# Optimization experiments

Measured on AMD Instinct MI355X. Metric: run time of the kernel, lower is better.

## Reference

```python
import jax, jax.numpy as jnp
import numpy as np

N = 50000      # nodes
E_RAND = 600000  # random edges per meta-path
M = 3          # meta-paths
D_IN = 128
D_OUT = 128
H_SEM = 128    # SemanticAttention hidden (default 128)
NEG_SLOPE = 0.2  # DGL GATConv leaky_relu default


def setup_inputs() -> dict:
    key = jax.random.key(0)
    ks = jax.random.split(key, 12)
    h = jax.random.normal(ks[0], (N, D_IN), dtype=jnp.float32)
    src = jax.random.randint(ks[1], (M, E_RAND), 0, N, dtype=jnp.int32)
    dst = jax.random.randint(ks[2], (M, E_RAND), 0, N, dtype=jnp.int32)
    # add self-loops (dgl.add_self_loop): guarantees every dst has >=1 edge
    loops = jnp.broadcast_to(jnp.arange(N, dtype=jnp.int32), (M, N))
    edge_src = jnp.concatenate([src, loops], axis=1)
    edge_dst = jnp.concatenate([dst, loops], axis=1)
    W_gat = jax.random.normal(ks[3], (M, D_IN, D_OUT), dtype=jnp.float32) * 0.05
    attn_l = jax.random.normal(ks[4], (M, D_OUT), dtype=jnp.float32) * 0.1
    attn_r = jax.random.normal(ks[5], (M, D_OUT), dtype=jnp.float32) * 0.1
    bias_gat = jax.random.normal(ks[6], (M, D_OUT), dtype=jnp.float32) * 0.02
    Ws1 = jax.random.normal(ks[7], (D_OUT, H_SEM), dtype=jnp.float32) * 0.05
    bs1 = jnp.zeros((H_SEM,), dtype=jnp.float32)
    Ws2 = jax.random.normal(ks[8], (H_SEM,), dtype=jnp.float32) * 0.05
    return {"h": h, "edge_src": edge_src, "edge_dst": edge_dst,
            "W_gat": W_gat, "attn_l": attn_l, "attn_r": attn_r,
            "bias_gat": bias_gat, "Ws1": Ws1, "bs1": bs1, "Ws2": Ws2}


def _gat_meta_path(feat_m, el_m, er_m, src, dst):
    # feat_m: [N, D]; el/er: [N]; src/dst: [E]
    e = jax.nn.leaky_relu(el_m[src] + er_m[dst], NEG_SLOPE)  # [E]
    emax = jax.ops.segment_max(e, dst, num_segments=N)       # [N]
    ex = jnp.exp(e - emax[dst])
    denom = jax.ops.segment_sum(ex, dst, num_segments=N)     # [N]
    a = ex / denom[dst]                                      # edge softmax
    # scatter-aggregate weighted source features -> [N, D]
    return jax.ops.segment_sum(a[:, None] * feat_m[src], dst, num_segments=N)


def reference(h, edge_src, edge_dst, W_gat, attn_l, attn_r, bias_gat, Ws1, bs1, Ws2):
    # per-meta-path GATConv projections
    feat = jnp.einsum('ni,mio->mno', h, W_gat)            # [M, N, D]
    el = jnp.einsum('mno,mo->mn', feat, attn_l)           # [M, N]
    er = jnp.einsum('mno,mo->mn', feat, attn_r)           # [M, N]
    z = jax.vmap(_gat_meta_path)(feat, el, er, edge_src, edge_dst)  # [M, N, D]
    z = jax.nn.elu(z + bias_gat[:, None, :])              # GATConv bias + activation
    z = jnp.transpose(z, (1, 0, 2))                       # [N, M, D]
    # SemanticAttention: Linear -> tanh -> Linear(no bias), mean over nodes, softmax over meta-paths
    w = jnp.einsum('nmh,h->nm', jnp.tanh(jnp.einsum('nmd,dh->nmh', z, Ws1) + bs1), Ws2)
    beta = jax.nn.softmax(w.mean(0))                      # [M]
    return jnp.einsum('m,nmd->nd', beta, z)               # [N, D]
```

## Files before the change

kernel.cpp:

```cpp
#include <hip/hip_runtime.h>
#include <hip/hip_fp16.h>

#define NV 50000
#define EE 650000
#define MM 3
#define NBUK 49
#define CHSZ 4096
#define NCH 159
#define SEMBLK 586

typedef __attribute__((ext_vector_type(8))) __bf16 bf16x8;
typedef __attribute__((ext_vector_type(8))) unsigned short u16x8;
typedef __attribute__((ext_vector_type(4))) float f32x4;

__device__ __forceinline__ unsigned short f2bf(float f) {
    unsigned u = __builtin_bit_cast(unsigned, f);
    u += 0x7FFFu + ((u >> 16) & 1u);
    return (unsigned short)(u >> 16);
}
__device__ __forceinline__ float bflo(unsigned v) {
    unsigned x = v << 16; return __builtin_bit_cast(float, x);
}
__device__ __forceinline__ float bfhi(unsigned v) {
    unsigned x = v & 0xFFFF0000u; return __builtin_bit_cast(float, x);
}
__device__ __forceinline__ bf16x8 zero8() {
    u16x8 u = {0,0,0,0,0,0,0,0};
    return __builtin_bit_cast(bf16x8, u);
}

__global__ void prep_wt(const float* __restrict__ Wg, const float* __restrict__ Ws1,
                        unsigned short* __restrict__ WT, unsigned short* __restrict__ WsT) {
    int idx = blockIdx.x * 256 + threadIdx.x;
    if (idx < MM * 16384) {
        int m = idx / 16384, r = idx % 16384;
        int o = r >> 7, d = r & 127;
        WT[idx] = f2bf(Wg[m * 16384 + d * 128 + o]);
    } else {
        int r = idx - MM * 16384;
        int j = r >> 7, d = r & 127;
        WsT[r] = f2bf(Ws1[d * 128 + j]);
    }
}

__global__ void prep_h(const float* __restrict__ h, unsigned* __restrict__ hb) {
    int idx = blockIdx.x * 256 + threadIdx.x;
    if (idx < NV * 64) {
        float2 f = *reinterpret_cast<const float2*>(h + (size_t)idx * 2);
        hb[idx] = ((unsigned)f2bf(f.x)) | (((unsigned)f2bf(f.y)) << 16);
    }
}

__global__ __launch_bounds__(256, 2) void gemm_feat(
    const unsigned short* __restrict__ hb, const unsigned short* __restrict__ WT,
    const float* __restrict__ attn_l, const float* __restrict__ attn_r,
    unsigned* __restrict__ featb, float* __restrict__ el, float* __restrict__ er) {
    const int m = blockIdx.y;
    const int tid = threadIdx.x;
    const int wave = tid >> 6, lane = tid & 63;
    const int lo = lane & 15, hi = lane >> 4;
    const int rowbase = blockIdx.x * 256 + wave * 64;
    const unsigned short* WTm = WT + m * 16384;

    f32x4 acc[4][8];
#pragma unroll
    for (int a = 0; a < 4; ++a)
#pragma unroll
        for (int b = 0; b < 8; ++b) acc[a][b] = (f32x4){0.f, 0.f, 0.f, 0.f};

#pragma unroll
    for (int kk = 0; kk < 4; ++kk) {
        bf16x8 bfrag[8];
#pragma unroll
        for (int ct = 0; ct < 8; ++ct)
            bfrag[ct] = *reinterpret_cast<const bf16x8*>(WTm + (ct * 16 + lo) * 128 + kk * 32 + hi * 8);
#pragma unroll
        for (int rt = 0; rt < 4; ++rt) {
            int row = rowbase + rt * 16 + lo;
            bf16x8 af = (row < NV)
                ? *reinterpret_cast<const bf16x8*>(hb + (size_t)row * 128 + kk * 32 + hi * 8)
                : zero8();
#pragma unroll
            for (int ct = 0; ct < 8; ++ct)
                acc[rt][ct] = __builtin_amdgcn_mfma_f32_16x16x32_bf16(af, bfrag[ct], acc[rt][ct], 0, 0, 0);
        }
    }

    float alv[8], arv[8];
#pragma unroll
    for (int ct = 0; ct < 8; ++ct) {
        alv[ct] = attn_l[m * 128 + ct * 16 + lo];
        arv[ct] = attn_r[m * 128 + ct * 16 + lo];
    }

#pragma unroll
    for (int rt = 0; rt < 4; ++rt) {
        float pl[4] = {0.f, 0.f, 0.f, 0.f}, pr[4] = {0.f, 0.f, 0.f, 0.f};
#pragma unroll
        for (int ct = 0; ct < 8; ++ct)
#pragma unroll
            for (int i = 0; i < 4; ++i) {
                pl[i] += acc[rt][ct][i] * alv[ct];
                pr[i] += acc[rt][ct][i] * arv[ct];
            }
#pragma unroll
        for (int s = 1; s < 16; s <<= 1)
#pragma unroll
            for (int i = 0; i < 4; ++i) {
                pl[i] += __shfl_xor(pl[i], s, 64);
                pr[i] += __shfl_xor(pr[i], s, 64);
            }
        int row0 = rowbase + rt * 16 + hi * 4;
        if (lo == 0) {
#pragma unroll
            for (int i = 0; i < 4; ++i)
                if (row0 + i < NV) {
                    el[m * NV + row0 + i] = pl[i];
                    er[m * NV + row0 + i] = pr[i];
                }
        }
#pragma unroll
        for (int ct = 0; ct < 8; ++ct)
#pragma unroll
            for (int i = 0; i < 4; ++i) {
                float v = acc[rt][ct][i];
                float vp = __shfl_xor(v, 1, 64);
                int row = row0 + i;
                if (((lo & 1) == 0) && row < NV) {
                    unsigned pk = ((unsigned)f2bf(v)) | (((unsigned)f2bf(vp)) << 16);
                    featb[(size_t)(m * NV + row) * 64 + ct * 8 + (lo >> 1)] = pk;
                }
            }
    }
}

__global__ __launch_bounds__(256) void hist_k(const int* __restrict__ edst,
                                              int* __restrict__ counts) {
    int m = blockIdx.y, c = blockIdx.x, tid = threadIdx.x;
    __shared__ int hsm[NBUK];
    if (tid < NBUK) hsm[tid] = 0;
    __syncthreads();
    int base = c * CHSZ;
#pragma unroll
    for (int i = 0; i < CHSZ / 256; ++i) {
        int e = base + i * 256 + tid;
        if (e < EE) {
            int d = edst[(size_t)m * EE + e];
            atomicAdd(&hsm[d >> 10], 1);
        }
    }
    __syncthreads();
    if (tid < NBUK) counts[(m * NCH + c) * NBUK + tid] = hsm[tid];
}

__global__ __launch_bounds__(256) void scan_k(const int* __restrict__ counts,
                                              int* __restrict__ chunkpos,
                                              int* __restrict__ bstart) {
    int t = threadIdx.x;
    __shared__ int btot[MM * NBUK];
    if (t < MM * NBUK) {
        int m = t / NBUK, b = t % NBUK;
        int run = 0;
        for (int c = 0; c < NCH; ++c) {
            chunkpos[(m * NCH + c) * NBUK + b] = run;
            run += counts[(m * NCH + c) * NBUK + b];
        }
        btot[t] = run;
    }
    __syncthreads();
    if (t == 0) {
        for (int m = 0; m < MM; ++m) {
            int run = 0;
            for (int b = 0; b < NBUK; ++b) {
                bstart[m * NBUK + b] = run;
                run += btot[m * NBUK + b];
            }
        }
    }
}

__global__ __launch_bounds__(256) void scat1_k(const int* __restrict__ esrc,
                                               const int* __restrict__ edst,
                                               const int* __restrict__ chunkpos,
                                               const int* __restrict__ bstart,
                                               unsigned* __restrict__ staging) {
    int m = blockIdx.y, c = blockIdx.x, tid = threadIdx.x;
    __shared__ int cnt[NBUK];
    __shared__ int sofs[NBUK];
    if (tid < NBUK) {
        cnt[tid] = 0;
        sofs[tid] = bstart[m * NBUK + tid] + chunkpos[(m * NCH + c) * NBUK + tid];
    }
    __syncthreads();
    int base = c * CHSZ;
#pragma unroll
    for (int i = 0; i < CHSZ / 256; ++i) {
        int e = base + i * 256 + tid;
        if (e < EE) {
            int s = esrc[(size_t)m * EE + e];
            int d = edst[(size_t)m * EE + e];
            int b = d >> 10;
            int r = atomicAdd(&cnt[b], 1);
            staging[(size_t)m * EE + sofs[b] + r] =
                ((unsigned)(d & 1023) << 16) | (unsigned)s;
        }
    }
}

__global__ __launch_bounds__(1024) void bsort_k(const unsigned* __restrict__ staging,
                                                const int* __restrict__ bstart,
                                                const float* __restrict__ el,
                                                const float* __restrict__ er,
                                                unsigned* __restrict__ csr,
                                                int* __restrict__ start,
                                                int* __restrict__ deg) {
    int b = blockIdx.x, m = blockIdx.y, t = threadIdx.x;
    __shared__ int hsm[1024];
    __shared__ int sc[1024];
    __shared__ int cur[1024];
    hsm[t] = 0;
    __syncthreads();
    int sbase = bstart[m * NBUK + b];
    int nseg = ((b == NBUK - 1) ? EE : bstart[m * NBUK + b + 1]) - sbase;
    const unsigned* sp = staging + (size_t)m * EE + sbase;
    for (int i = t; i < nseg; i += 1024)
        atomicAdd(&hsm[sp[i] >> 16], 1);
    __syncthreads();
    int v = hsm[t];
    sc[t] = v;
    __syncthreads();
#pragma unroll
    for (int s = 1; s < 1024; s <<= 1) {
        int add = (t >= s) ? sc[t - s] : 0;
        __syncthreads();
        sc[t] += add;
        __syncthreads();
    }
    int excl = sc[t] - v;
    cur[t] = excl;
    int node = (b << 10) + t;
    if (node < NV) {
        deg[m * NV + node] = v;
        start[m * NV + node] = sbase + excl;
    }
    __syncthreads();
    unsigned* cp = csr + (size_t)m * EE + sbase;
    int node0 = b << 10;
    for (int i = t; i < nseg; i += 1024) {
        unsigned rec = sp[i];
        int dloc = rec >> 16;
        int s = rec & 0xFFFF;
        float x = el[m * NV + s] + er[m * NV + node0 + dloc];
        x = x > 0.f ? x : 0.2f * x;
        float ex = __expf(x);
        unsigned short hx = __builtin_bit_cast(unsigned short, __float2half(ex));
        int slot = atomicAdd(&cur[dloc], 1);
        cp[slot] = ((unsigned)hx << 16) | (unsigned)s;
    }
}

__global__ __launch_bounds__(256) void aggregate_k(
    const unsigned* __restrict__ featb, const unsigned* __restrict__ csr,
    const int* __restrict__ start, const int* __restrict__ deg,
    const float* __restrict__ bias, float* __restrict__ z, unsigned* __restrict__ zb) {
    int gw = blockIdx.x * 4 + (threadIdx.x >> 6);
    int lane = threadIdx.x & 63;
    int m = gw / NV;
    int st = start[gw];
    int dg = deg[gw];
    const unsigned* pp = csr + (size_t)m * EE + st;
    const unsigned* fb = featb + (size_t)m * NV * 64 + lane;
    float2 acc = {0.f, 0.f};
    float den = 0.f;
    int full = dg & ~7;
    int e0 = 0;
    for (; e0 < full; e0 += 8) {
        unsigned p[8];
#pragma unroll
        for (int i = 0; i < 8; ++i) p[i] = pp[e0 + i];
        unsigned v[8];
#pragma unroll
        for (int i = 0; i < 8; ++i) v[i] = fb[(size_t)(p[i] & 0xFFFF) * 64];
#pragma unroll
        for (int i = 0; i < 8; ++i) {
            float x = __half2float(__builtin_bit_cast(__half, (unsigned short)(p[i] >> 16)));
            acc.x += x * bflo(v[i]); acc.y += x * bfhi(v[i]);
            den += x;
        }
    }
    if (e0 < dg) {
        int dgm1 = dg - 1;
        unsigned p[8];
#pragma unroll
        for (int i = 0; i < 8; ++i) p[i] = pp[min(e0 + i, dgm1)];
        unsigned v[8];
#pragma unroll
        for (int i = 0; i < 8; ++i) v[i] = fb[(size_t)(p[i] & 0xFFFF) * 64];
#pragma unroll
        for (int i = 0; i < 8; ++i) {
            float x = (e0 + i < dg)
                ? __half2float(__builtin_bit_cast(__half, (unsigned short)(p[i] >> 16))) : 0.f;
            acc.x += x * bflo(v[i]); acc.y += x * bfhi(v[i]);
            den += x;
        }
    }
    float inv = 1.f / den;
    int d0 = lane * 2;
    float z0 = acc.x * inv + bias[m * 128 + d0];
    float z1 = acc.y * inv + bias[m * 128 + d0 + 1];
    z0 = z0 > 0.f ? z0 : (__expf(z0) - 1.f);
    z1 = z1 > 0.f ? z1 : (__expf(z1) - 1.f);
    float2 o = {z0, z1};
    *reinterpret_cast<float2*>(z + (size_t)gw * 128 + d0) = o;
    zb[(size_t)gw * 64 + lane] = ((unsigned)f2bf(z0)) | (((unsigned)f2bf(z1)) << 16);
}

__global__ __launch_bounds__(256, 2) void semantic_k(
    const unsigned* __restrict__ zb, const unsigned short* __restrict__ WsT,
    const float* __restrict__ bs1, const float* __restrict__ Ws2,
    float* __restrict__ wpart) {
    const int tid = threadIdx.x;
    const int wave = tid >> 6, lane = tid & 63;
    const int lo = lane & 15, hi = lane >> 4;
    const int rowbase = blockIdx.x * 256 + wave * 64;

    f32x4 acc[4][8];
#pragma unroll
    for (int a = 0; a < 4; ++a)
#pragma unroll
        for (int b = 0; b < 8; ++b) acc[a][b] = (f32x4){0.f, 0.f, 0.f, 0.f};

#pragma unroll
    for (int kk = 0; kk < 4; ++kk) {
        bf16x8 bfrag[8];
#pragma unroll
        for (int ct = 0; ct < 8; ++ct)
            bfrag[ct] = *reinterpret_cast<const bf16x8*>(WsT + (ct * 16 + lo) * 128 + kk * 32 + hi * 8);
#pragma unroll
        for (int rt = 0; rt < 4; ++rt) {
            int row = rowbase + rt * 16 + lo;
            bf16x8 af = (row < MM * NV)
                ? *reinterpret_cast<const bf16x8*>(zb + (size_t)row * 64 + kk * 16 + hi * 2)
                : zero8();
#pragma unroll
            for (int ct = 0; ct < 8; ++ct)
                acc[rt][ct] = __builtin_amdgcn_mfma_f32_16x16x32_bf16(af, bfrag[ct], acc[rt][ct], 0, 0, 0);
        }
    }

    float w2v[8], b1v[8];
#pragma unroll
    for (int ct = 0; ct < 8; ++ct) {
        w2v[ct] = Ws2[ct * 16 + lo];
        b1v[ct] = bs1[ct * 16 + lo];
    }

    float t0 = 0.f, t1 = 0.f, t2 = 0.f;
#pragma unroll
    for (int rt = 0; rt < 4; ++rt) {
        int rbase = rowbase + rt * 16;
        if (rbase >= MM * NV) continue;
        int mm = rbase / NV;
        float p = 0.f;
#pragma unroll
        for (int ct = 0; ct < 8; ++ct)
#pragma unroll
            for (int i = 0; i < 4; ++i) {
                float x = acc[rt][ct][i] + b1v[ct];
                x = fminf(fmaxf(x, -15.f), 15.f);
                float t = __expf(2.f * x);
                p += w2v[ct] * ((t - 1.f) / (t + 1.f));
            }
#pragma unroll
        for (int s = 1; s < 64; s <<= 1) p += __shfl_xor(p, s, 64);
        if (mm == 0) t0 += p; else if (mm == 1) t1 += p; else t2 += p;
    }

    __shared__ float smw[4][3];
    if (lane == 0) { smw[wave][0] = t0; smw[wave][1] = t1; smw[wave][2] = t2; }
    __syncthreads();
    if (tid < 3)
        wpart[blockIdx.x * 4 + tid] =
            smw[0][tid] + smw[1][tid] + smw[2][tid] + smw[3][tid];
}

__global__ __launch_bounds__(64) void beta_k(const float* __restrict__ wpart,
                                             float* __restrict__ beta) {
    int lane = threadIdx.x;
    float t0 = 0.f, t1 = 0.f, t2 = 0.f;
    for (int b = lane; b < SEMBLK; b += 64) {
        t0 += wpart[b * 4 + 0];
        t1 += wpart[b * 4 + 1];
        t2 += wpart[b * 4 + 2];
    }
#pragma unroll
    for (int s = 1; s < 64; s <<= 1) {
        t0 += __shfl_xor(t0, s, 64);
        t1 += __shfl_xor(t1, s, 64);
        t2 += __shfl_xor(t2, s, 64);
    }
    if (lane == 0) {
        float w0 = t0 * (1.f / NV), w1 = t1 * (1.f / NV), w2 = t2 * (1.f / NV);
        float mx = fmaxf(w0, fmaxf(w1, w2));
        float e0 = __expf(w0 - mx), e1 = __expf(w1 - mx), e2 = __expf(w2 - mx);
        float inv = 1.f / (e0 + e1 + e2);
        beta[0] = e0 * inv; beta[1] = e1 * inv; beta[2] = e2 * inv;
    }
}

__global__ __launch_bounds__(256) void combine_k(const float* __restrict__ z,
                                                 const float* __restrict__ beta,
                                                 float* __restrict__ out) {
    size_t base = (size_t)(blockIdx.x * 256 + threadIdx.x) * 4;
    float b0 = beta[0], b1 = beta[1], b2 = beta[2];
    float4 z0 = *reinterpret_cast<const float4*>(z + base);
    float4 z1 = *reinterpret_cast<const float4*>(z + (size_t)NV * 128 + base);
    float4 z2 = *reinterpret_cast<const float4*>(z + (size_t)2 * NV * 128 + base);
    float4 o;
    o.x = b0 * z0.x + b1 * z1.x + b2 * z2.x;
    o.y = b0 * z0.y + b1 * z1.y + b2 * z2.y;
    o.z = b0 * z0.z + b1 * z1.z + b2 * z2.z;
    o.w = b0 * z0.w + b1 * z1.w + b2 * z2.w;
    *reinterpret_cast<float4*>(out + base) = o;
}

extern "C" void kernel_launch(void* const* d_in, const int* in_sizes, int n_in,
                              void* d_out, int out_size, void* d_ws, size_t ws_size,
                              hipStream_t stream) {
    const float* h      = (const float*)d_in[0];
    const int*   esrc   = (const int*)d_in[1];
    const int*   edst   = (const int*)d_in[2];
    const float* Wg     = (const float*)d_in[3];
    const float* attn_l = (const float*)d_in[4];
    const float* attn_r = (const float*)d_in[5];
    const float* bias   = (const float*)d_in[6];
    const float* Ws1    = (const float*)d_in[7];
    const float* bs1    = (const float*)d_in[8];
    const float* Ws2    = (const float*)d_in[9];
    float* out = (float*)d_out;

    char* w = (char*)d_ws;
    auto alloc = [&](size_t bytes) { char* p = w; w += (bytes + 255) & ~(size_t)255; return p; };
    unsigned short* WT   = (unsigned short*)alloc((size_t)MM * 128 * 128 * 2);
    unsigned short* WsT  = (unsigned short*)alloc((size_t)128 * 128 * 2);
    unsigned* hb    = (unsigned*)alloc((size_t)NV * 64 * 4);
    unsigned* featb = (unsigned*)alloc((size_t)MM * NV * 64 * 4);
    unsigned* zbp   = (unsigned*)alloc((size_t)MM * NV * 64 * 4);
    float* zbuf   = (float*)alloc((size_t)MM * NV * 128 * 4);
    float* el     = (float*)alloc((size_t)MM * NV * 4);
    float* er     = (float*)alloc((size_t)MM * NV * 4);
    int*   deg    = (int*)alloc((size_t)MM * NV * 4);
    int*   startb = (int*)alloc((size_t)MM * NV * 4);
    int*   counts = (int*)alloc((size_t)MM * NCH * NBUK * 4);
    int*   chunkpos = (int*)alloc((size_t)MM * NCH * NBUK * 4);
    int*   bstart = (int*)alloc((size_t)MM * NBUK * 4);
    unsigned* staging = (unsigned*)alloc((size_t)MM * EE * 4);
    unsigned* csr     = (unsigned*)alloc((size_t)MM * EE * 4);
    float* wpart  = (float*)alloc((size_t)SEMBLK * 4 * 4);
    float* beta   = (float*)alloc(256);

    hipLaunchKernelGGL(prep_wt, dim3(256), dim3(256), 0, stream, Wg, Ws1, WT, WsT);
    hipLaunchKernelGGL(prep_h, dim3((NV * 64 + 255) / 256), dim3(256), 0, stream, h, hb);
    hipLaunchKernelGGL(gemm_feat, dim3(196, MM), dim3(256), 0, stream,
                       (const unsigned short*)hb, WT, attn_l, attn_r, featb, el, er);
    hipLaunchKernelGGL(hist_k, dim3(NCH, MM), dim3(256), 0, stream, edst, counts);
    hipLaunchKernelGGL(scan_k, dim3(1), dim3(256), 0, stream, counts, chunkpos, bstart);
    hipLaunchKernelGGL(scat1_k, dim3(NCH, MM), dim3(256), 0, stream,
                       esrc, edst, chunkpos, bstart, staging);
    hipLaunchKernelGGL(bsort_k, dim3(NBUK, MM), dim3(1024), 0, stream,
                       staging, bstart, el, er, csr, startb, deg);
    hipLaunchKernelGGL(aggregate_k, dim3((MM * NV) / 4), dim3(256), 0, stream,
                       featb, csr, startb, deg, bias, zbuf, zbp);
    hipLaunchKernelGGL(semantic_k, dim3(SEMBLK), dim3(256), 0, stream,
                       zbp, WsT, bs1, Ws2, wpart);
    hipLaunchKernelGGL(beta_k, dim3(1), dim3(64), 0, stream, wpart, beta);
    hipLaunchKernelGGL(combine_k, dim3(6250), dim3(256), 0, stream, zbuf, beta, out);
}
```

Baseline: 255.2 us.

## Store aggregated z once as fp16 and use half-wave per node aggregation

Replaces the separate fp32 z buffer and bf16 copy with a single fp16 z buffer, which semantic attention (now f16 MFMA) and combine both read. This cuts the large fp32 write and reread of z. Aggregation now maps two nodes per wave, each lane gathering 8 bytes per source row instead of 4, to widen the gathers. The cost is fp16 precision in the final output and possible overflow if z grows large.

```diff
diff --git a/kernel.cpp b/kernel.cpp
--- a/kernel.cpp
+++ b/kernel.cpp
@@ -10,6 +10,7 @@
 #define SEMBLK 586
 
 typedef __attribute__((ext_vector_type(8))) __bf16 bf16x8;
+typedef __attribute__((ext_vector_type(8))) _Float16 f16x8;
 typedef __attribute__((ext_vector_type(8))) unsigned short u16x8;
 typedef __attribute__((ext_vector_type(4))) float f32x4;
 
@@ -27,6 +28,16 @@
 __device__ __forceinline__ bf16x8 zero8() {
     u16x8 u = {0,0,0,0,0,0,0,0};
     return __builtin_bit_cast(bf16x8, u);
+}
+__device__ __forceinline__ f16x8 zero8h() {
+    u16x8 u = {0,0,0,0,0,0,0,0};
+    return __builtin_bit_cast(f16x8, u);
+}
+__device__ __forceinline__ unsigned short f2h(float f) {
+    return __builtin_bit_cast(unsigned short, __float2half(f));
+}
+__device__ __forceinline__ float h2f(unsigned short u) {
+    return __half2float(__builtin_bit_cast(__half, u));
 }
 
 __global__ void prep_wt(const float* __restrict__ Wg, const float* __restrict__ Ws1,
@@ -39,7 +50,7 @@
     } else {
         int r = idx - MM * 16384;
         int j = r >> 7, d = r & 127;
-        WsT[r] = f2bf(Ws1[d * 128 + j]);
+        WsT[r] = f2h(Ws1[d * 128 + j]);
     }
 }
 
@@ -253,24 +264,24 @@
         float x = el[m * NV + s] + er[m * NV + node0 + dloc];
         x = x > 0.f ? x : 0.2f * x;
         float ex = __expf(x);
-        unsigned short hx = __builtin_bit_cast(unsigned short, __float2half(ex));
         int slot = atomicAdd(&cur[dloc], 1);
-        cp[slot] = ((unsigned)hx << 16) | (unsigned)s;
+        cp[slot] = ((unsigned)f2h(ex) << 16) | (unsigned)s;
     }
 }
 
 __global__ __launch_bounds__(256) void aggregate_k(
     const unsigned* __restrict__ featb, const unsigned* __restrict__ csr,
     const int* __restrict__ start, const int* __restrict__ deg,
-    const float* __restrict__ bias, float* __restrict__ z, unsigned* __restrict__ zb) {
-    int gw = blockIdx.x * 4 + (threadIdx.x >> 6);
-    int lane = threadIdx.x & 63;
+    const float* __restrict__ bias, unsigned* __restrict__ zh) {
+    int wid = blockIdx.x * 4 + (threadIdx.x >> 6);
+    int gw = wid * 2 + ((threadIdx.x >> 5) & 1);
+    int sl = threadIdx.x & 31;
     int m = gw / NV;
     int st = start[gw];
     int dg = deg[gw];
     const unsigned* pp = csr + (size_t)m * EE + st;
-    const unsigned* fb = featb + (size_t)m * NV * 64 + lane;
-    float2 acc = {0.f, 0.f};
+    const unsigned* fb = featb + (size_t)m * NV * 64 + sl * 2;
+    float2 a01 = {0.f, 0.f}, a23 = {0.f, 0.f};
     float den = 0.f;
     int full = dg & ~7;
     int e0 = 0;
@@ -278,13 +289,15 @@
         unsigned p[8];
 #pragma unroll
         for (int i = 0; i < 8; ++i) p[i] = pp[e0 + i];
-        unsigned v[8];
-#pragma unroll
-        for (int i = 0; i < 8; ++i) v[i] = fb[(size_t)(p[i] & 0xFFFF) * 64];
+        uint2 v[8];
+#pragma unroll
+        for (int i = 0; i < 8; ++i)
+            v[i] = *reinterpret_cast<const uint2*>(fb + (size_t)(p[i] & 0xFFFF) * 64);
 #pragma unroll
         for (int i = 0; i < 8; ++i) {
-            float x = __half2float(__builtin_bit_cast(__half, (unsigned short)(p[i] >> 16)));
-            acc.x += x * bflo(v[i]); acc.y += x * bfhi(v[i]);
+            float x = h2f((unsigned short)(p[i] >> 16));
+            a01.x += x * bflo(v[i].x); a01.y += x * bfhi(v[i].x);
+            a23.x += x * bflo(v[i].y); a23.y += x * bfhi(v[i].y);
             den += x;
         }
     }
@@ -293,30 +306,37 @@
         unsigned p[8];
 #pragma unroll
         for (int i = 0; i < 8; ++i) p[i] = pp[min(e0 + i, dgm1)];
-        unsigned v[8];
-#pragma unroll
-        for (int i = 0; i < 8; ++i) v[i] = fb[(size_t)(p[i] & 0xFFFF) * 64];
+        uint2 v[8];
+#pragma unroll
+        for (int i = 0; i < 8; ++i)
+            v[i] = *reinterpret_cast<const uint2*>(fb + (size_t)(p[i] & 0xFFFF) * 64);
 #pragma unroll
         for (int i = 0; i < 8; ++i) {
-            float x = (e0 + i < dg)
-                ? __half2float(__builtin_bit_cast(__half, (unsigned short)(p[i] >> 16))) : 0.f;
-            acc.x += x * bflo(v[i]); acc.y += x * bfhi(v[i]);
+            float x = (e0 + i < dg) ? h2f((unsigned short)(p[i] >> 16)) : 0.f;
+            a01.x += x * bflo(v[i].x); a01.y += x * bfhi(v[i].x);
+            a23.x += x * bflo(v[i].y); a23.y += x * bfhi(v[i].y);
             den += x;
         }
     }
     float inv = 1.f / den;
-    int d0 = lane * 2;
-    float z0 = acc.x * inv + bias[m * 128 + d0];
-    float z1 = acc.y * inv + bias[m * 128 + d0 + 1];
+    int d0 = sl * 4;
+    const float* bp = bias + m * 128 + d0;
+    float z0 = a01.x * inv + bp[0];
+    float z1 = a01.y * inv + bp[1];
+    float z2 = a23.x * inv + bp[2];
+    float z3 = a23.y * inv + bp[3];
     z0 = z0 > 0.f ? z0 : (__expf(z0) - 1.f);
     z1 = z1 > 0.f ? z1 : (__expf(z1) - 1.f);
-    float2 o = {z0, z1};
-    *reinterpret_cast<float2*>(z + (size_t)gw * 128 + d0) = o;
-    zb[(size_t)gw * 64 + lane] = ((unsigned)f2bf(z0)) | (((unsigned)f2bf(z1)) << 16);
+    z2 = z2 > 0.f ? z2 : (__expf(z2) - 1.f);
+    z3 = z3 > 0.f ? z3 : (__expf(z3) - 1.f);
+    uint2 o;
+    o.x = ((unsigned)f2h(z0)) | (((unsigned)f2h(z1)) << 16);
+    o.y = ((unsigned)f2h(z2)) | (((unsigned)f2h(z3)) << 16);
+    *reinterpret_cast<uint2*>(zh + (size_t)gw * 64 + sl * 2) = o;
 }
 
 __global__ __launch_bounds__(256, 2) void semantic_k(
-    const unsigned* __restrict__ zb, const unsigned short* __restrict__ WsT,
+    const unsigned* __restrict__ zh, const unsigned short* __restrict__ WsT,
     const float* __restrict__ bs1, const float* __restrict__ Ws2,
     float* __restrict__ wpart) {
     const int tid = threadIdx.x;
@@ -332,19 +352,19 @@
 
 #pragma unroll
     for (int kk = 0; kk < 4; ++kk) {
-        bf16x8 bfrag[8];
+        f16x8 bfrag[8];
 #pragma unroll
         for (int ct = 0; ct < 8; ++ct)
-            bfrag[ct] = *reinterpret_cast<const bf16x8*>(WsT + (ct * 16 + lo) * 128 + kk * 32 + hi * 8);
+            bfrag[ct] = *reinterpret_cast<const f16x8*>(WsT + (ct * 16 + lo) * 128 + kk * 32 + hi * 8);
 #pragma unroll
         for (int rt = 0; rt < 4; ++rt) {
             int row = rowbase + rt * 16 + lo;
-            bf16x8 af = (row < MM * NV)
-                ? *reinterpret_cast<const bf16x8*>(zb + (size_t)row * 64 + kk * 16 + hi * 2)
-                : zero8();
+            f16x8 af = (row < MM * NV)
+                ? *reinterpret_cast<const f16x8*>(zh + (size_t)row * 64 + kk * 16 + hi * 2)
+                : zero8h();
 #pragma unroll
             for (int ct = 0; ct < 8; ++ct)
-                acc[rt][ct] = __builtin_amdgcn_mfma_f32_16x16x32_bf16(af, bfrag[ct], acc[rt][ct], 0, 0, 0);
+                acc[rt][ct] = __builtin_amdgcn_mfma_f32_16x16x32_f16(af, bfrag[ct], acc[rt][ct], 0, 0, 0);
         }
     }
 
@@ -408,20 +428,26 @@
     }
 }
 
-__global__ __launch_bounds__(256) void combine_k(const float* __restrict__ z,
+__global__ __launch_bounds__(256) void combine_k(const unsigned* __restrict__ zh,
                                                  const float* __restrict__ beta,
                                                  float* __restrict__ out) {
-    size_t base = (size_t)(blockIdx.x * 256 + threadIdx.x) * 4;
+    int idx = blockIdx.x * 256 + threadIdx.x;
     float b0 = beta[0], b1 = beta[1], b2 = beta[2];
-    float4 z0 = *reinterpret_cast<const float4*>(z + base);
-    float4 z1 = *reinterpret_cast<const float4*>(z + (size_t)NV * 128 + base);
-    float4 z2 = *reinterpret_cast<const float4*>(z + (size_t)2 * NV * 128 + base);
+    uint2 u0 = *reinterpret_cast<const uint2*>(zh + (size_t)idx * 2);
+    uint2 u1 = *reinterpret_cast<const uint2*>(zh + (size_t)NV * 64 + (size_t)idx * 2);
+    uint2 u2 = *reinterpret_cast<const uint2*>(zh + (size_t)2 * NV * 64 + (size_t)idx * 2);
+    float2 a0 = __half22float2(__builtin_bit_cast(__half2, u0.x));
+    float2 a1 = __half22float2(__builtin_bit_cast(__half2, u0.y));
+    float2 c0 = __half22float2(__builtin_bit_cast(__half2, u1.x));
+    float2 c1 = __half22float2(__builtin_bit_cast(__half2, u1.y));
+    float2 d0 = __half22float2(__builtin_bit_cast(__half2, u2.x));
+    float2 d1 = __half22float2(__builtin_bit_cast(__half2, u2.y));
     float4 o;
-    o.x = b0 * z0.x + b1 * z1.x + b2 * z2.x;
-    o.y = b0 * z0.y + b1 * z1.y + b2 * z2.y;
-    o.z = b0 * z0.z + b1 * z1.z + b2 * z2.z;
-    o.w = b0 * z0.w + b1 * z1.w + b2 * z2.w;
-    *reinterpret_cast<float4*>(out + base) = o;
+    o.x = b0 * a0.x + b1 * c0.x + b2 * d0.x;
+    o.y = b0 * a0.y + b1 * c0.y + b2 * d0.y;
+    o.z = b0 * a1.x + b1 * c1.x + b2 * d1.x;
+    o.w = b0 * a1.y + b1 * c1.y + b2 * d1.y;
+    *reinterpret_cast<float4*>(out + (size_t)idx * 4) = o;
 }
 
 extern "C" void kernel_launch(void* const* d_in, const int* in_sizes, int n_in,
@@ -445,8 +471,7 @@
     unsigned short* WsT  = (unsigned short*)alloc((size_t)128 * 128 * 2);
     unsigned* hb    = (unsigned*)alloc((size_t)NV * 64 * 4);
     unsigned* featb = (unsigned*)alloc((size_t)MM * NV * 64 * 4);
-    unsigned* zbp   = (unsigned*)alloc((size_t)MM * NV * 64 * 4);
-    float* zbuf   = (float*)alloc((size_t)MM * NV * 128 * 4);
+    unsigned* zh    = (unsigned*)alloc((size_t)MM * NV * 64 * 4);
     float* el     = (float*)alloc((size_t)MM * NV * 4);
     float* er     = (float*)alloc((size_t)MM * NV * 4);
     int*   deg    = (int*)alloc((size_t)MM * NV * 4);
@@ -469,10 +494,10 @@
                        esrc, edst, chunkpos, bstart, staging);
     hipLaunchKernelGGL(bsort_k, dim3(NBUK, MM), dim3(1024), 0, stream,
                        staging, bstart, el, er, csr, startb, deg);
-    hipLaunchKernelGGL(aggregate_k, dim3((MM * NV) / 4), dim3(256), 0, stream,
-                       featb, csr, startb, deg, bias, zbuf, zbp);
+    hipLaunchKernelGGL(aggregate_k, dim3((MM * NV) / 8), dim3(256), 0, stream,
+                       featb, csr, startb, deg, bias, zh);
     hipLaunchKernelGGL(semantic_k, dim3(SEMBLK), dim3(256), 0, stream,
-                       zbp, WsT, bs1, Ws2, wpart);
+                       zh, WsT, bs1, Ws2, wpart);
     hipLaunchKernelGGL(beta_k, dim3(1), dim3(64), 0, stream, wpart, beta);
-    hipLaunchKernelGGL(combine_k, dim3(6250), dim3(256), 0, stream, zbuf, beta, out);
-}
+    hipLaunchKernelGGL(combine_k, dim3(6250), dim3(256), 0, stream, zh, beta, out);
+}
```

Result: faster. 233.5 us (-8.5%).
